# Performance work log

Hardware: AMD Instinct MI355X
Metric: run time of the kernel (lower is better)

Reference implementation:

```python
import jax, jax.numpy as jnp
import numpy as np

B = 4; IN_CH = 256; HEAD_CH = 64; NUM_CLS = 3; H = 128; W = 128
NH = 4; KEY = 16; VAL = 16; OUT_CH = 2
VX = 0.1 * 8; VY = 0.1 * 8  # voxel_size[:2] * out_size_factor
DW = 1.6; DL = 3.9; STRIDE = 1
C_CTR = (HEAD_CH + 2 + NUM_CLS) * 9      # 621
C_COR = (HEAD_CH + 2 + NUM_CLS * 4) * 8  # 624
C_FG = (HEAD_CH + 2 + NUM_CLS) * 9       # 621


def _sampler_points():
    offs = np.arange(-STRIDE, STRIDE + 1, STRIDE, dtype=np.float32)
    oy, ox = np.meshgrid(offs, offs, indexing='ij')
    ctr = np.stack([ox, oy], 0).reshape(2, 9)  # pixel offsets
    cx = np.array([-DW/2, -DW/2, DW/2, DW/2, DL/2, -DL/2, DL/2, -DL/2], np.float32) / VX
    cy = np.array([DL/2, -DL/2, DL/2, -DL/2, -DW/2, -DW/2, DW/2, DW/2], np.float32) / VY
    # faithful to torch: stack(dim=1) -> [8,2] then .view(2,8) (row-major reinterpret)
    cor = np.stack([cx, cy], 1).reshape(2, 8)
    r = max(DW, DL)
    fx = np.array([-r/3, -r/3, -r/3, 0, 0, 0, r/3, r/3, r/3], np.float32) / VX
    fy = np.array([-r/3, 0, r/3, -r/3, 0, r/3, -r/3, 0, r/3], np.float32) / VY
    fg = np.stack([fx, fy], 1).reshape(2, 9)
    return jnp.asarray(ctr), jnp.asarray(cor), jnp.asarray(fg)


def _raw_grid():
    gx = jnp.arange(W, dtype=jnp.float32) + 0.5
    gy = jnp.arange(H, dtype=jnp.float32) + 0.5
    return jnp.stack([jnp.broadcast_to(gx[None, :], (H, W)),
                      jnp.broadcast_to(gy[:, None], (H, W))], 0)  # [2,H,W]


def _conv3x3(x, w, b):
    y = jax.lax.conv_general_dilated(x, w, (1, 1), 'SAME',
                                     dimension_numbers=('NCHW', 'OIHW', 'NCHW'))
    return y + b[None, :, None, None]


def _cbr3(x, w, b, s, t):  # conv3x3 + inference-mode BN (folded scale/shift) + relu
    return jax.nn.relu(_conv3x3(x, w, b) * s[None, :, None, None] + t[None, :, None, None])


def _cbr1(x, w, b, s, t):  # per-head 1x1 conv + BN + relu, w: [NH,O,C], x: [B,C,H,W]
    y = jnp.einsum('noc,bchw->nbohw', w, x) + b[:, None, :, None, None]
    return jax.nn.relu(y * s[:, None, :, None, None] + t[:, None, :, None, None])


def _sample(feats, grids):
    # feats [B,C,H,W]; grids [2,n,H,W] pixel coords. Matches F.grid_sample
    # (bilinear, zeros padding, align_corners=False): sample at pixel coord g-0.5.
    n = grids.shape[1]
    geo = jnp.stack([grids[0] / W, grids[1] / H], 0)  # recover_coords, [2,n,H,W]
    gx, gy = grids[0] - 0.5, grids[1] - 0.5
    x0f = jnp.floor(gx); y0f = jnp.floor(gy)
    dx, dy = gx - x0f, gy - y0f
    x0 = x0f.astype(jnp.int32); y0 = y0f.astype(jnp.int32)
    flat = feats.reshape(B, -1, H * W)

    def gather(xc, yc, wgt):
        valid = ((xc >= 0) & (xc < W) & (yc >= 0) & (yc < H)).astype(feats.dtype) * wgt
        idx = jnp.clip(yc, 0, H - 1) * W + jnp.clip(xc, 0, W - 1)
        v = jnp.take(flat, idx.reshape(-1), axis=2).reshape(B, -1, n, H, W)
        return v * valid[None, None]

    s = (gather(x0, y0, (1 - dx) * (1 - dy)) + gather(x0 + 1, y0, dx * (1 - dy))
         + gather(x0, y0 + 1, (1 - dx) * dy) + gather(x0 + 1, y0 + 1, dx * dy))
    geo_b = jnp.broadcast_to(geo[None], (B,) + geo.shape)
    out = jnp.concatenate([s, geo_b], axis=1)  # [B,C+2,n,H,W]
    return out.reshape(B, -1, H, W)           # channel index = c*n + p, as torch .view


def _forward(base_feats, cc_w, cc_b, cc_s, cc_t, ch_w, ch_b,
             oc_w, oc_b, oc_s, oc_t, oh_w, oh_b,
             fc_w, fc_b, fc_s, fc_t, fh_w, fh_b,
             q_w, q_b, q_s, q_t,
             ck_w, ck_b, ck_s, ck_t, cv_w, cv_b, cv_s, cv_t,
             kk_w, kk_b, kk_s, kk_t, kv_w, kv_b, kv_s, kv_t,
             fk_w, fk_b, fk_s, fk_t, fv_w, fv_b, fv_s, fv_t,
             p1_w, p1_b, p1_s, p1_t, p2_w, p2_b):
    center_feat = _cbr3(base_feats, cc_w, cc_b, cc_s, cc_t)
    center_map = _conv3x3(center_feat, ch_w, ch_b)
    corner_feat = _cbr3(base_feats, oc_w, oc_b, oc_s, oc_t)
    corner_map = _conv3x3(corner_feat, oh_w, oh_b)
    fg_feat = _cbr3(base_feats, fc_w, fc_b, fc_s, fc_t)
    fg_map = _conv3x3(fg_feat, fh_w, fh_b)

    ctr_pts, cor_pts, fg_pts = _sampler_points()
    raw = _raw_grid()
    g_ctr = raw[:, None] + ctr_pts[:, :, None, None]  # [2,9,H,W]
    g_cor = raw[:, None] + cor_pts[:, :, None, None]  # [2,8,H,W]
    g_fg = raw[:, None] + fg_pts[:, :, None, None]    # [2,9,H,W]

    cs = _sample(jnp.concatenate([center_feat, center_map], 1), g_ctr)  # [B,621,H,W]
    os_ = _sample(jnp.concatenate([corner_feat, corner_map], 1), g_cor)  # [B,624,H,W]
    fs = _sample(jnp.concatenate([fg_feat, fg_map], 1), g_fg)            # [B,621,H,W]

    q = _cbr1(base_feats, q_w, q_b, q_s, q_t)  # [NH,B,KEY,H,W]
    ck = _cbr1(cs, ck_w, ck_b, ck_s, ck_t); cv = _cbr1(cs, cv_w, cv_b, cv_s, cv_t)
    ok = _cbr1(os_, kk_w, kk_b, kk_s, kk_t); ov = _cbr1(os_, kv_w, kv_b, kv_s, kv_t)
    fk = _cbr1(fs, fk_w, fk_b, fk_s, fk_t); fv = _cbr1(fs, fv_w, fv_b, fv_s, fv_t)

    logits = jnp.stack([(q * ck).sum(2), (q * ok).sum(2), (q * fk).sum(2)], axis=2)  # [NH,B,3,H,W]
    attw = jax.nn.softmax(logits, axis=2)
    vals = jnp.stack([cv, ov, fv], axis=2)          # [NH,B,3,VAL,H,W]
    att = (attw[:, :, :, None] * vals).sum(2)       # [NH,B,VAL,H,W]

    # predict: 1x1 conv over cat([base_feats, att]) + BN + relu, then 1x1 to out_ch
    h1 = (jnp.einsum('noc,bchw->nbohw', p1_w[:, :, :IN_CH], base_feats)
          + jnp.einsum('nov,nbvhw->nbohw', p1_w[:, :, IN_CH:], att)
          + p1_b[:, None, :, None, None])
    h1 = jax.nn.relu(h1 * p1_s[:, None, :, None, None] + p1_t[:, None, :, None, None])
    pred = jnp.einsum('npo,nbohw->nbphw', p2_w, h1) + p2_b[:, None, :, None, None]
    heads = jnp.moveaxis(pred, 0, 1).reshape(B, NH * OUT_CH, H, W)
    return jnp.concatenate([center_map, corner_map, fg_map, heads], axis=1)  # [B,26,H,W]


def setup_inputs() -> dict:
    ks = iter(jax.random.split(jax.random.key(0), 80))

    def rn(shape, s=0.05):
        return jax.random.normal(next(ks), shape, jnp.float32) * s

    d = {"base_feats": jax.random.normal(next(ks), (B, IN_CH, H, W), jnp.float32)}
    for conv, head, hc in (("cc", "ch", NUM_CLS), ("oc", "oh", NUM_CLS * 4), ("fc", "fh", NUM_CLS)):
        d[conv + "_w"] = rn((HEAD_CH, IN_CH, 3, 3)); d[conv + "_b"] = rn((HEAD_CH,))
        d[conv + "_s"] = 1.0 + rn((HEAD_CH,)); d[conv + "_t"] = rn((HEAD_CH,))
        d[head + "_w"] = rn((hc, HEAD_CH, 3, 3)); d[head + "_b"] = jnp.full((hc,), -2.19, jnp.float32)
    d["q_w"] = rn((NH, KEY, IN_CH)); d["q_b"] = rn((NH, KEY))
    d["q_s"] = 1.0 + rn((NH, KEY)); d["q_t"] = rn((NH, KEY))
    for name, cin, cout in (("ck", C_CTR, KEY), ("cv", C_CTR, VAL), ("kk", C_COR, KEY),
                            ("kv", C_COR, VAL), ("fk", C_FG, KEY), ("fv", C_FG, VAL)):
        d[name + "_w"] = rn((NH, cout, cin)); d[name + "_b"] = rn((NH, cout))
        d[name + "_s"] = 1.0 + rn((NH, cout)); d[name + "_t"] = rn((NH, cout))
    d["p1_w"] = rn((NH, HEAD_CH, IN_CH + VAL)); d["p1_b"] = rn((NH, HEAD_CH))
    d["p1_s"] = 1.0 + rn((NH, HEAD_CH)); d["p1_t"] = rn((NH, HEAD_CH))
    d["p2_w"] = rn((NH, OUT_CH, HEAD_CH)); d["p2_b"] = jnp.full((NH, OUT_CH), -2.19, jnp.float32)
    return d


def reference(base_feats, cc_w, cc_b, cc_s, cc_t, ch_w, ch_b,
              oc_w, oc_b, oc_s, oc_t, oh_w, oh_b,
              fc_w, fc_b, fc_s, fc_t, fh_w, fh_b,
              q_w, q_b, q_s, q_t,
              ck_w, ck_b, ck_s, ck_t, cv_w, cv_b, cv_s, cv_t,
              kk_w, kk_b, kk_s, kk_t, kv_w, kv_b, kv_s, kv_t,
              fk_w, fk_b, fk_s, fk_t, fv_w, fv_b, fv_s, fv_t,
              p1_w, p1_b, p1_s, p1_t, p2_w, p2_b):
    return _forward(base_feats, cc_w, cc_b, cc_s, cc_t, ch_w, ch_b,
                    oc_w, oc_b, oc_s, oc_t, oh_w, oh_b,
                    fc_w, fc_b, fc_s, fc_t, fh_w, fh_b,
                    q_w, q_b, q_s, q_t,
                    ck_w, ck_b, ck_s, ck_t, cv_w, cv_b, cv_s, cv_t,
                    kk_w, kk_b, kk_s, kk_t, kv_w, kv_b, kv_s, kv_t,
                    fk_w, fk_b, fk_s, fk_t, fv_w, fv_b, fv_s, fv_t,
                    p1_w, p1_b, p1_s, p1_t, p2_w, p2_b)
```

## Files before the change

### kernel.cpp

```cpp
#include <hip/hip_runtime.h>
#include <hip/hip_bf16.h>
#include <math.h>


#define HW 16384
#define WIMG 128

typedef unsigned short ushortT;
typedef __attribute__((ext_vector_type(8))) short short8;
typedef __attribute__((ext_vector_type(4))) float floatx4;
typedef __attribute__((ext_vector_type(4))) unsigned uintx4;

constexpr size_t OFF_KV    = 16777216;
constexpr size_t OFF_A16   = 29360128;
constexpr size_t OFF_B16   = 38012928;
constexpr size_t OFF_CWT   = 46057216;
constexpr size_t OFF_CB    = OFF_CWT + 221184;
constexpr size_t OFF_HWT   = OFF_CB + 192;
constexpr size_t OFF_QWT   = OFF_HWT + 13824;
constexpr size_t OFF_QB    = OFF_QWT + 8192;
constexpr size_t OFF_KVW   = OFF_QB + 64;
constexpr size_t OFF_GEO   = OFF_KVW + 266240;
constexpr size_t OFF_P1WT  = OFF_GEO + 1152;
constexpr size_t OFF_P1B   = OFF_P1WT + 40960;

struct P53 { const float* p[53]; };

__device__ inline ushortT f2bf(float f) {
    unsigned u = __float_as_uint(f);
    unsigned r = (u + 0x7FFFu + ((u >> 16) & 1u)) >> 16;
    return (ushortT)r;
}
__device__ inline unsigned packbf(float a, float b) {
    return (unsigned)f2bf(a) | ((unsigned)f2bf(b) << 16);
}
__device__ inline float bf2f(ushortT u) {
    return __uint_as_float((unsigned)u << 16);
}

typedef __attribute__((address_space(3))) ushortT lds_us;
typedef __attribute__((address_space(1))) const ushortT glb_us;
__device__ inline void gload_lds16(const ushortT* g, ushortT* ldsbase) {
    __builtin_amdgcn_global_load_lds((glb_us*)g, (lds_us*)ldsbase, 16, 0, 0);
}

__device__ const float c_ox[3][9] = {
    {-1.f, 0.f, 1.f, -1.f, 0.f, 1.f, -1.f, 0.f, 1.f},
    {-1.f, 2.4375f, -1.f, -2.4375f, 1.f, 2.4375f, 1.f, -2.4375f, 0.f},
    {-1.625f, -1.625f, -1.625f, 0.f, -1.625f, 1.625f, 0.f, -1.625f, 0.f}};
__device__ const float c_oy[3][9] = {
    {-1.f, -1.f, -1.f, 0.f, 0.f, 0.f, 1.f, 1.f, 1.f},
    {2.4375f, -1.f, -2.4375f, -1.f, 2.4375f, 1.f, -2.4375f, 1.f, 0.f},
    {0.f, 0.f, 1.625f, 1.625f, -1.625f, 1.625f, 0.f, 1.625f, 1.625f}};

__device__ const int tapX_cor[16] = {-1,-1, 2, 3,-1,-1,-3,-2, 1, 1, 2, 3, 1, 1,-3,-2};
__device__ const int tapY_cor[16] = { 2, 3,-1,-1,-3,-2,-1,-1, 2, 3, 1, 1,-3,-2, 1, 1};
__device__ const int tapR_cor[16] = { 4, 5, 2, 2, 0, 1, 2, 2, 4, 5, 3, 3, 0, 1, 3, 3};

__device__ inline float cornw(float off, int X) {
    float f = floorf(off);
    float d = off - f;
    int fi = (int)f;
    return (X == fi) ? (1.f - d) : (X == fi + 1) ? d : 0.f;
}

__global__ __launch_bounds__(256) void setup_kernel(P53 ptrs, float* __restrict__ ws,
                                                    const float* __restrict__ base,
                                                    ushortT* __restrict__ a16,
                                                    ushortT* __restrict__ b16) {
    int i = blockIdx.x * 256 + threadIdx.x;
    const float* const* p = ptrs.p;
    if (i < 1102464) {
        if (i < 442368) {
            int tap = i / 49152, r = i % 49152;
            int g = r / 1536, r2 = r % 1536;
            int M = r2 >> 3, j = r2 & 7;
            int br = M >> 6, oc = M & 63, ic = g * 8 + j;
            float v = p[1 + 6 * br][(oc * 256 + ic) * 9 + tap] * p[3 + 6 * br][oc];
            ((ushortT*)(ws + OFF_CWT))[i] = f2bf(v);
            return;
        }
        i -= 442368;
        if (i < 192) {
            int br = i >> 6, oc = i & 63;
            ws[OFF_CB + i] = p[2 + 6 * br][oc] * p[3 + 6 * br][oc] + p[4 + 6 * br][oc];
            return;
        }
        i -= 192;
        if (i < 27648) {
            int j = i & 7, m = (i >> 3) & 15, u = (i >> 7) % 72, br = i / 9216;
            int cnt = (br == 1) ? 12 : 3;
            int t = u >> 3, g = u & 7, ic = g * 8 + j;
            const float* hw = (br == 0) ? p[5] : (br == 1) ? p[11] : p[17];
            float v = (m < cnt) ? hw[(m * 64 + ic) * 9 + t] : 0.f;
            ((ushortT*)(ws + OFF_HWT))[i] = f2bf(v);
            return;
        }
        i -= 27648;
        if (i < 16384) {
            int j = i & 7, m = (i >> 3) & 63, sg = i >> 9;
            int k = (sg >> 2) * 32 + (sg & 3) * 8 + j;
            ((ushortT*)(ws + OFF_QWT))[i] = f2bf(p[19][m * 256 + k] * p[21][m]);
            return;
        }
        i -= 16384;
        if (i < 64) { ws[OFF_QB + i] = p[20][i] * p[21][i] + p[22][i]; return; }
        i -= 64;
        if (i < 532480) {
            int br, NQ, NTAP, n, C, i2;
            if (i < 110592)      { br = 0; NQ = 3; NTAP = 9;  n = 9; C = 67; i2 = i; }
            else if (i < 274432) { br = 1; NQ = 4; NTAP = 16; n = 8; C = 76; i2 = i - 110592; }
            else                 { br = 2; NQ = 7; NTAP = 25; n = 9; C = 67; i2 = i - 274432; }
            int gsz = NQ * 4096;
            int g = i2 / gsz, r = i2 % gsz;
            int q = r >> 12, r2 = r & 4095;
            int sub = r2 >> 10, m = (r2 >> 3) & 127, j = r2 & 7;
            int t = q * 4 + sub, c = g * 8 + j;
            float v = 0.f;
            if (t < NTAP && c < C) {
                int X, Y;
                if (br == 0)      { X = t % 3 - 1; Y = t / 3 - 1; }
                else if (br == 1) { X = tapX_cor[t]; Y = tapY_cor[t]; }
                else              { X = t % 5 - 2; Y = t / 5 - 2; }
                const float* wsrc = (m < 64) ? p[23 + 8 * br] : p[27 + 8 * br];
                int mo = (m < 64) ? m : m - 64;
                float sc = (m < 64) ? p[25 + 8 * br][mo] : p[29 + 8 * br][mo];
                int Cn = (C + 2) * n;
                float s = 0.f;
                for (int pp = 0; pp < n; ++pp) {
                    float ww = cornw(c_ox[br][pp], X) * cornw(c_oy[br][pp], Y);
                    if (ww != 0.f) s += ww * wsrc[mo * Cn + c * n + pp];
                }
                v = s * sc;
            }
            ((ushortT*)(ws + OFF_KVW))[i] = f2bf(v);
            return;
        }
        i -= 532480;
        if (i < 1152) {
            int br = i / 384, rem = i % 384, which = rem >> 7, m = rem & 127;
            int n = (br == 1) ? 8 : 9, C = (br == 1) ? 76 : 67, Cn = (C + 2) * n;
            const float* wsrc = (m < 64) ? p[23 + 8 * br] : p[27 + 8 * br];
            int mo = (m < 64) ? m : m - 64;
            float sc = (m < 64) ? p[25 + 8 * br][mo] : p[29 + 8 * br][mo];
            float bb = (m < 64) ? p[24 + 8 * br][mo] : p[28 + 8 * br][mo];
            float tt = (m < 64) ? p[26 + 8 * br][mo] : p[30 + 8 * br][mo];
            float v = 0.f;
            if (which == 0) {
                for (int pp = 0; pp < n; ++pp) v += wsrc[mo * Cn + C * n + pp];
                v *= sc;
            } else if (which == 1) {
                for (int pp = 0; pp < n; ++pp) v += wsrc[mo * Cn + (C + 1) * n + pp];
                v *= sc;
            } else {
                for (int pp = 0; pp < n; ++pp)
                    v += wsrc[mo * Cn + C * n + pp] * c_ox[br][pp]
                       + wsrc[mo * Cn + (C + 1) * n + pp] * c_oy[br][pp];
                v = v * sc * 0.0078125f + bb * sc + tt;
            }
            ws[OFF_GEO + br * 384 + which * 128 + m] = v;
            return;
        }
        i -= 1152;
        if (i < 81920) {
            int j = i & 7, M = (i >> 3) & 255, sg = i >> 11;
            int k = (sg >> 2) * 32 + (sg & 3) * 8 + j;
            int nh = M >> 6, oc = M & 63;
            float sc = p[49][nh * 64 + oc];
            float v;
            if (k < 256) v = p[47][(nh * 64 + oc) * 272 + k] * sc;
            else {
                int k2 = k - 256, nh2 = k2 >> 4, va = k2 & 15;
                v = (nh2 == nh) ? p[47][(nh * 64 + oc) * 272 + 256 + va] * sc : 0.f;
            }
            ((ushortT*)(ws + OFF_P1WT))[i] = f2bf(v);
            return;
        }
        i -= 81920;
        if (i < 256) { ws[OFF_P1B + i] = p[48][i] * p[49][i] + p[50][i]; }
        return;
    }
    int idx = i - 1102464;
    if (idx < 4 * 32 * 130 * 130) {
        int col = idx % 130, t = idx / 130;
        int row = t % 130; t /= 130;
        int icg = t & 31, b = t >> 5;
        int h = row - 1, w = col - 1;
        unsigned wds[4] = {0u, 0u, 0u, 0u};
        if ((unsigned)h < 128u && (unsigned)w < 128u) {
            const float* s = base + (size_t)(b * 256 + icg * 8) * HW + h * WIMG + w;
            #pragma unroll
            for (int jp = 0; jp < 4; ++jp)
                wds[jp] = packbf(s[(size_t)(2 * jp) * HW], s[(size_t)(2 * jp + 1) * HW]);
        }
        unsigned* d = (unsigned*)(a16 + (size_t)idx * 8);
        d[0] = wds[0]; d[1] = wds[1]; d[2] = wds[2]; d[3] = wds[3];
        return;
    }
    idx -= 4 * 32 * 130 * 130;
    if (idx < 4 * 28 * 134 * 134) {
        int col = idx % 134, row = (idx / 134) % 134;
        if (row < 3 || row >= 131 || col < 3 || col >= 131) {
            unsigned* d = (unsigned*)(b16 + (size_t)idx * 8);
            d[0] = 0u; d[1] = 0u; d[2] = 0u; d[3] = 0u;
        }
    }
}

__global__ __launch_bounds__(256) void conv_base_mfma(
    const ushortT* __restrict__ a16, const ushortT* __restrict__ wA,
    const float* __restrict__ cb, ushortT* __restrict__ b16)
{
    const int wv = threadIdx.x >> 6, lane = threadIdx.x & 63;
    const int sub = lane >> 4, ln = lane & 15;
    const int xh = blockIdx.x, h = blockIdx.y, b = blockIdx.z;
    const int x0 = xh * 64;
    __shared__ __align__(16) ushortT sbuf[2][792 * 8];

    floatx4 acc[3][4];
    #pragma unroll
    for (int mt = 0; mt < 3; ++mt)
        #pragma unroll
        for (int nt = 0; nt < 4; ++nt)
            #pragma unroll
            for (int r = 0; r < 4; ++r) acc[mt][nt][r] = 0.f;

    const int wbase = threadIdx.x & ~63;
    auto stage = [&](int s, int buf) {
        #pragma unroll
        for (int it = 0; it < 4; ++it) {
            int idx = threadIdx.x + it * 256;
            if (idx < 792) {
                int col = idx % 66, t2 = idx / 66;
                int r = t2 % 3, icg = t2 / 3;
                const ushortT* g = a16 +
                    (((size_t)(b * 32 + s * 4 + icg) * 130 + (h + r)) * 130 + (x0 + col)) * 8;
                gload_lds16(g, &sbuf[buf][(size_t)(it * 256 + wbase) * 8]);
            }
        }
    };
    stage(0, 0);
    for (int s = 0; s < 8; ++s) {
        __syncthreads();
        if (s < 7) stage(s + 1, (s + 1) & 1);
        const ushortT* sb = sbuf[s & 1];
        #pragma unroll
        for (int tap = 0; tap < 9; ++tap) {
            const int ky = tap / 3, kx = tap % 3;
            short8 Bf[4];
            #pragma unroll
            for (int nt = 0; nt < 4; ++nt) {
                int c = nt * 16 + ln + kx;
                Bf[nt] = *(const short8*)(sb + ((sub * 3 + ky) * 66 + c) * 8);
            }
            const int g = s * 4 + sub;
            short8 Af[3];
            #pragma unroll
            for (int mt = 0; mt < 3; ++mt) {
                int m = wv * 48 + mt * 16 + ln;
                Af[mt] = *(const short8*)(wA + (((size_t)tap * 32 + g) * 192 + m) * 8);
            }
            #pragma unroll
            for (int mt = 0; mt < 3; ++mt)
                #pragma unroll
                for (int nt = 0; nt < 4; ++nt)
                    acc[mt][nt] = __builtin_amdgcn_mfma_f32_16x16x32_bf16(
                        Af[mt], Bf[nt], acc[mt][nt], 0, 0, 0);
        }
    }
    #pragma unroll
    for (int mt = 0; mt < 3; ++mt) {
        int ocq = wv * 48 + mt * 16 + sub * 4;
        #pragma unroll
        for (int nt = 0; nt < 4; ++nt) {
            int px = x0 + nt * 16 + ln;
            float v0 = fmaxf(acc[mt][nt][0] + cb[ocq + 0], 0.f);
            float v1 = fmaxf(acc[mt][nt][1] + cb[ocq + 1], 0.f);
            float v2 = fmaxf(acc[mt][nt][2] + cb[ocq + 2], 0.f);
            float v3 = fmaxf(acc[mt][nt][3] + cb[ocq + 3], 0.f);
            unsigned lo = packbf(v0, v1), hi = packbf(v2, v3);
            unsigned plo = (unsigned)__shfl_down((int)lo, 16);
            unsigned phi = (unsigned)__shfl_down((int)hi, 16);
            if (!(sub & 1)) {
                int br = ocq >> 6, oc = ocq & 63;
                int grp = ((br == 0) ? 0 : (br == 1) ? 9 : 19) + (oc >> 3);
                uintx4 w = {lo, hi, plo, phi};
                *(uintx4*)(b16 +
                    (((size_t)(b * 28 + grp) * 134 + (h + 3)) * 134 + (px + 3)) * 8) = w;
            }
        }
    }
}

__global__ __launch_bounds__(256) void conv_head_mfma(
    const ushortT* __restrict__ b16c, const ushortT* __restrict__ wH,
    const float* __restrict__ chb, const float* __restrict__ ohb,
    const float* __restrict__ fhb, float* __restrict__ out,
    ushortT* __restrict__ b16)
{
    const int wv = threadIdx.x >> 6, lane = threadIdx.x & 63;
    const int sub = lane >> 4, ln = lane & 15;
    const int x0 = (blockIdx.x & 1) * 64, h = blockIdx.x >> 1;
    const int br = blockIdx.y % 3, b = blockIdx.y / 3;
    const int cnt = (br == 1) ? 12 : 3;
    const int mapb = (br == 0) ? 0 : (br == 1) ? 3 : 15;
    const int grpb = (br == 0) ? 0 : (br == 1) ? 9 : 19;
    const float* bias = (br == 0) ? chb : (br == 1) ? ohb : fhb;
    __shared__ __align__(16) ushortT sbuf[8 * 3 * 66 * 8];
    const int wbase = threadIdx.x & ~63;

    for (int it = 0; it < 7; ++it) {
        int idx = threadIdx.x + it * 256;
        if (idx < 1584) {
            int col = idx % 66, t2 = idx / 66;
            int r = t2 % 3, g = t2 / 3;
            const ushortT* gp = b16c +
                (((size_t)(b * 28 + grpb + g) * 134 + (h + r + 2)) * 134 + (x0 + col + 2)) * 8;
            gload_lds16(gp, sbuf + (size_t)(it * 256 + wbase) * 8);
        }
    }
    __syncthreads();

    floatx4 acc;
    #pragma unroll
    for (int r = 0; r < 4; ++r) acc[r] = 0.f;
    #pragma unroll
    for (int k = 0; k < 18; ++k) {
        int u = k * 4 + sub;
        int t = u >> 3, g = u & 7;
        int dxv = t % 3 - 1, ry = t / 3;
        short8 Af = *(const short8*)(wH + ((size_t)(br * 72 + u) * 16 + ln) * 8);
        int c = wv * 16 + ln + dxv + 1;
        short8 Bf = *(const short8*)(sbuf + ((g * 3 + ry) * 66 + c) * 8);
        acc = __builtin_amdgcn_mfma_f32_16x16x32_bf16(Af, Bf, acc, 0, 0, 0);
    }
    {
        int px = x0 + wv * 16 + ln;
        #pragma unroll
        for (int r = 0; r < 4; ++r) {
            int m = sub * 4 + r;
            if (m < cnt) {
                float v = acc[r] + bias[m];
                out[((size_t)b * 26 + mapb + m) * HW + h * WIMG + px] = v;
                int grp = grpb + 8 + (m >> 3), j = m & 7;
                b16[(((size_t)(b * 28 + grp) * 134 + (h + 3)) * 134 + (px + 3)) * 8 + j]
                    = f2bf(v);
            }
        }
    }
}

template<int BRV>
__device__ __forceinline__ void kv_body(
    const ushortT* __restrict__ b16, const ushortT* __restrict__ kvw,
    const float* __restrict__ geob, ushortT* __restrict__ kvout,
    ushortT* __restrict__ sbuf)
{
    constexpr int NGRP = (BRV == 0) ? 9 : (BRV == 1) ? 5 : 9;
    constexpr int NPH  = (BRV == 1) ? 2 : 1;
    constexpr int NTAP = (BRV == 0) ? 9 : (BRV == 1) ? 16 : 25;
    constexpr int NQ   = (BRV == 0) ? 3 : (BRV == 1) ? 4 : 7;
    constexpr int ROWS = (BRV == 0) ? 3 : (BRV == 1) ? 6 : 5;
    constexpr int COLS = (BRV == 0) ? 34 : (BRV == 1) ? 38 : 36;
    constexpr int XMIN = (BRV == 0) ? -1 : (BRV == 1) ? -3 : -2;
    constexpr int UBASE = (BRV == 0) ? 0 : (BRV == 1) ? 9 : 19;
    constexpr int NEL  = NGRP * ROWS * COLS;
    constexpr int NIT  = (NEL + 255) / 256;
    constexpr int WBASE = (BRV == 0) ? 0 : (BRV == 1) ? 110592 : 274432;

    const int lane = threadIdx.x & 63, wv = threadIdx.x >> 6;
    const int sub = lane >> 4, ln = lane & 15;
    const int x0 = blockIdx.x * 32, h = blockIdx.y;
    const int b = blockIdx.z & 3;
    const int wbase = threadIdx.x & ~63;
    const int thrB = ln * 16;

    int boff[NQ];
    #pragma unroll
    for (int q = 0; q < NQ; ++q) {
        int t = q * 4 + sub;
        int dxv, ry;
        if (t >= NTAP)          { dxv = -XMIN; ry = 0; }
        else if (BRV == 0)      { dxv = t % 3 - 1; ry = t / 3; }
        else if (BRV == 1)      { dxv = tapX_cor[t]; ry = tapR_cor[t]; }
        else                    { dxv = t % 5 - 2; ry = t / 5; }
        boff[q] = (ry * COLS + (dxv - XMIN)) * 16 + thrB;
    }

    auto stage = [&](int ph) {
        #pragma unroll
        for (int it = 0; it < NIT; ++it) {
            int idx = threadIdx.x + it * 256;
            if (idx < NEL) {
                int grp = idx / (ROWS * COLS), r2 = idx % (ROWS * COLS);
                int rw = r2 / COLS, col = r2 % COLS;
                int dy = (BRV == 1) ? ((rw < 3) ? rw - 3 : rw - 2) : (rw - ROWS / 2);
                const ushortT* gp = b16 +
                    (((size_t)(b * 28 + UBASE + ph * NGRP + grp) * 134 + (h + dy + 3)) * 134
                     + (x0 + col + XMIN + 3)) * 8;
                gload_lds16(gp, sbuf + (size_t)(it * 256 + wbase) * 8);
            }
        }
    };

    floatx4 acc[2][2];
    #pragma unroll
    for (int mt = 0; mt < 2; ++mt)
        #pragma unroll
        for (int nt = 0; nt < 2; ++nt)
            #pragma unroll
            for (int r = 0; r < 4; ++r) acc[mt][nt][r] = 0.f;

    for (int ph = 0; ph < NPH; ++ph) {
        if (ph) __syncthreads();
        stage(ph);
        __syncthreads();
        for (int g = 0; g < NGRP; ++g) {
            const char* sb8 = (const char*)sbuf + g * (ROWS * COLS * 16);
            const ushortT* wg = kvw + WBASE
                + ((size_t)(ph * NGRP + g) * NQ) * 4096 + sub * 1024 + (wv * 32 + ln) * 8;
            short8 A0[2], B0[2], A1[2], B1[2];
            auto ldf = [&](int q, short8 A[2], short8 B[2]) {
                #pragma unroll
                for (int mt = 0; mt < 2; ++mt)
                    A[mt] = *(const short8*)(wg + (size_t)q * 4096 + mt * 128);
                int bb = boff[q];
                #pragma unroll
                for (int nt = 0; nt < 2; ++nt)
                    B[nt] = *(const short8*)(sb8 + bb + nt * 256);
            };
            auto dom = [&](short8 A[2], short8 B[2]) {
                #pragma unroll
                for (int mt = 0; mt < 2; ++mt)
                    #pragma unroll
                    for (int nt = 0; nt < 2; ++nt)
                        acc[mt][nt] = __builtin_amdgcn_mfma_f32_16x16x32_bf16(
                            A[mt], B[nt], acc[mt][nt], 0, 0, 0);
            };
            ldf(0, A0, B0);
            #pragma unroll
            for (int q = 0; q < NQ; q += 2) {
                bool h1 = (q + 1 < NQ);
                if (h1) ldf(q + 1, A1, B1);
                dom(A0, B0);
                if (q + 2 < NQ) ldf(q + 2, A0, B0);
                if (h1) dom(A1, B1);
            }
        }
    }

    const float* geo = geob + BRV * 384;
    const float fy = (h + 0.5f) * 0.0078125f;
    #pragma unroll
    for (int mt = 0; mt < 2; ++mt)
        #pragma unroll
        for (int nt = 0; nt < 2; ++nt) {
            int px = x0 + nt * 16 + ln;
            float fx = (px + 0.5f) * 0.0078125f;
            #pragma unroll
            for (int r = 0; r < 4; ++r) {
                int Mi = wv * 32 + mt * 16 + sub * 4 + r;
                float v = acc[mt][nt][r] + geo[Mi] * fx + geo[128 + Mi] * fy + geo[256 + Mi];
                kvout[((size_t)(BRV * 4 + b) * 128 + Mi) * HW + h * WIMG + px] =
                    f2bf(fmaxf(v, 0.f));
            }
        }
}

__global__ __launch_bounds__(256, 6) void kv_all3(
    const ushortT* __restrict__ b16, const ushortT* __restrict__ kvw,
    const float* __restrict__ geob, ushortT* __restrict__ kvout)
{
    __shared__ __align__(16) ushortT sbuf[1620 * 8];
    const int brv = blockIdx.z >> 2;
    if (brv == 0)      kv_body<0>(b16, kvw, geob, kvout, sbuf);
    else if (brv == 1) kv_body<1>(b16, kvw, geob, kvout, sbuf);
    else               kv_body<2>(b16, kvw, geob, kvout, sbuf);
}

__global__ __launch_bounds__(256) void attn_pred_mfma(
    float* __restrict__ ws, const float* __restrict__ p2w,
    const float* __restrict__ p2b, float* __restrict__ out)
{
    const int wv = threadIdx.x >> 6, lane = threadIdx.x & 63;
    const int sub = lane >> 4, ln = lane & 15;
    const int px0 = blockIdx.x * 64, b = blockIdx.y;
    const ushortT* wP1 = (const ushortT*)(ws + OFF_P1WT);
    const ushortT* wQ  = (const ushortT*)(ws + OFF_QWT);
    const ushortT* a16 = (const ushortT*)(ws + OFF_A16);
    const ushortT* kv = (const ushortT*)(ws + OFF_KV);
    const float* p1b = ws + OFF_P1B;
    const float* qb  = ws + OFF_QB;
    __shared__ __align__(16) ushortT xbuf[40 * 64 * 8];
    __shared__ __align__(16) ushortT qld[64 * 64];

    const int mypx = threadIdx.x & 63, nh = threadIdx.x >> 6;
    const int gpx = px0 + mypx, hh = gpx >> 7, ww = gpx & 127;
    #pragma unroll
    for (int g2 = 0; g2 < 8; ++g2) {
        int g = nh * 8 + g2;
        const ushortT* gp = a16 +
            (((size_t)(b * 32 + g) * 130 + (hh + 1)) * 130 + (ww + 1)) * 8;
        gload_lds16(gp, xbuf + (size_t)g * 64 * 8);
    }
    __syncthreads();

    {
        floatx4 qacc[4];
        #pragma unroll
        for (int nt = 0; nt < 4; ++nt)
            #pragma unroll
            for (int r = 0; r < 4; ++r) qacc[nt][r] = 0.f;
        #pragma unroll
        for (int kk = 0; kk < 8; ++kk) {
            short8 Af = *(const short8*)(wQ + (((kk * 4 + sub) * 64) + wv * 16 + ln) * 8);
            #pragma unroll
            for (int nt = 0; nt < 4; ++nt) {
                short8 Bf = *(const short8*)(xbuf + (((kk * 4 + sub) * 64) + nt * 16 + ln) * 8);
                qacc[nt] = __builtin_amdgcn_mfma_f32_16x16x32_bf16(Af, Bf, qacc[nt], 0, 0, 0);
            }
        }
        #pragma unroll
        for (int nt = 0; nt < 4; ++nt)
            #pragma unroll
            for (int r = 0; r < 4; ++r) {
                int row = wv * 16 + sub * 4 + r;
                qld[row * 64 + nt * 16 + ln] = f2bf(fmaxf(qacc[nt][r] + qb[row], 0.f));
            }
    }
    __syncthreads();

    {
        float l[3];
        #pragma unroll
        for (int br = 0; br < 3; ++br) {
            float s = 0.f;
            #pragma unroll
            for (int ko = 0; ko < 16; ++ko)
                s = fmaf(bf2f(qld[(nh * 16 + ko) * 64 + mypx]),
                         bf2f(kv[(size_t)((br * 4 + b) * 128 + nh * 16 + ko) * HW + gpx]), s);
            l[br] = s;
        }
        float m = fmaxf(l[0], fmaxf(l[1], l[2]));
        float e0 = __expf(l[0] - m), e1 = __expf(l[1] - m), e2 = __expf(l[2] - m);
        float inv = 1.f / (e0 + e1 + e2);
        float aw0 = e0 * inv, aw1 = e1 * inv, aw2 = e2 * inv;
        #pragma unroll
        for (int vap = 0; vap < 8; ++vap) {
            int va0 = vap * 2, va1 = vap * 2 + 1;
            float a0 =
                aw0 * bf2f(kv[(size_t)((0 * 4 + b) * 128 + 64 + nh * 16 + va0) * HW + gpx]) +
                aw1 * bf2f(kv[(size_t)((1 * 4 + b) * 128 + 64 + nh * 16 + va0) * HW + gpx]) +
                aw2 * bf2f(kv[(size_t)((2 * 4 + b) * 128 + 64 + nh * 16 + va0) * HW + gpx]);
            float a1 =
                aw0 * bf2f(kv[(size_t)((0 * 4 + b) * 128 + 64 + nh * 16 + va1) * HW + gpx]) +
                aw1 * bf2f(kv[(size_t)((1 * 4 + b) * 128 + 64 + nh * 16 + va1) * HW + gpx]) +
                aw2 * bf2f(kv[(size_t)((2 * 4 + b) * 128 + 64 + nh * 16 + va1) * HW + gpx]);
            int g = 32 + nh * 2 + (vap >> 2), wo = vap & 3;
            ((unsigned*)xbuf)[(g * 64 + mypx) * 4 + wo] = packbf(a0, a1);
        }
    }
    __syncthreads();

    floatx4 acc[4][4];
    #pragma unroll
    for (int mt = 0; mt < 4; ++mt)
        #pragma unroll
        for (int nt = 0; nt < 4; ++nt)
            #pragma unroll
            for (int r = 0; r < 4; ++r) acc[mt][nt][r] = 0.f;
    #pragma unroll
    for (int kk = 0; kk < 10; ++kk) {
        short8 Bf[4];
        #pragma unroll
        for (int nt = 0; nt < 4; ++nt)
            Bf[nt] = *(const short8*)(xbuf + (((kk * 4 + sub) * 64) + nt * 16 + ln) * 8);
        #pragma unroll
        for (int mt = 0; mt < 4; ++mt) {
            short8 Af = *(const short8*)(wP1 +
                (((size_t)(kk * 4 + sub) * 256) + wv * 64 + mt * 16 + ln) * 8);
            #pragma unroll
            for (int nt = 0; nt < 4; ++nt)
                acc[mt][nt] = __builtin_amdgcn_mfma_f32_16x16x32_bf16(Af, Bf[nt], acc[mt][nt], 0, 0, 0);
        }
    }

    float po0[4] = {0.f, 0.f, 0.f, 0.f}, po1[4] = {0.f, 0.f, 0.f, 0.f};
    #pragma unroll
    for (int mt = 0; mt < 4; ++mt)
        #pragma unroll
        for (int r = 0; r < 4; ++r) {
            int oc = mt * 16 + sub * 4 + r;
            float bias = p1b[wv * 64 + oc];
            float w0 = p2w[(wv * 2 + 0) * 64 + oc];
            float w1 = p2w[(wv * 2 + 1) * 64 + oc];
            #pragma unroll
            for (int nt = 0; nt < 4; ++nt) {
                float hv = fmaxf(acc[mt][nt][r] + bias, 0.f);
                po0[nt] = fmaf(w0, hv, po0[nt]);
                po1[nt] = fmaf(w1, hv, po1[nt]);
            }
        }
    #pragma unroll
    for (int nt = 0; nt < 4; ++nt) {
        po0[nt] += __shfl_xor(po0[nt], 16);
        po0[nt] += __shfl_xor(po0[nt], 32);
        po1[nt] += __shfl_xor(po1[nt], 16);
        po1[nt] += __shfl_xor(po1[nt], 32);
    }
    if (sub == 0) {
        #pragma unroll
        for (int nt = 0; nt < 4; ++nt) {
            int px = px0 + nt * 16 + ln;
            out[((size_t)b * 26 + 18 + wv * 2 + 0) * HW + px] = po0[nt] + p2b[wv * 2 + 0];
            out[((size_t)b * 26 + 18 + wv * 2 + 1) * HW + px] = po1[nt] + p2b[wv * 2 + 1];
        }
    }
}

extern "C" void kernel_launch(void* const* d_in, const int* in_sizes, int n_in,
                              void* d_out, int out_size, void* d_ws, size_t ws_size,
                              hipStream_t stream) {
    (void)in_sizes; (void)n_in; (void)out_size; (void)ws_size;
    float* ws  = (float*)d_ws;
    float* out = (float*)d_out;
    const float* base = (const float*)d_in[0];
    P53 ptrs;
    for (int i = 0; i < 53; ++i) ptrs.p[i] = (const float*)d_in[i];

    ushortT* a16 = (ushortT*)(ws + OFF_A16);
    ushortT* b16 = (ushortT*)(ws + OFF_B16);
    ushortT* kvb = (ushortT*)(ws + OFF_KV);
    const ushortT* kvw = (const ushortT*)(ws + OFF_KVW);

    setup_kernel<<<20613, 256, 0, stream>>>(ptrs, ws, base, a16, b16);
    conv_base_mfma<<<dim3(2, 128, 4), 256, 0, stream>>>(
        a16, (const ushortT*)(ws + OFF_CWT), ws + OFF_CB, b16);
    conv_head_mfma<<<dim3(256, 12), 256, 0, stream>>>(
        b16, (const ushortT*)(ws + OFF_HWT),
        (const float*)d_in[6], (const float*)d_in[12], (const float*)d_in[18],
        out, b16);
    kv_all3<<<dim3(4, 128, 12), 256, 0, stream>>>(b16, kvw, ws + OFF_GEO, kvb);
    attn_pred_mfma<<<dim3(256, 4), 256, 0, stream>>>(ws, (const float*)d_in[51],
                                                     (const float*)d_in[52], out);
}
```

Before: 436.4 us.

## Widen kv kernel tile to full image row, stage one group at a time

The kv conv kernel now has each block compute a full 128-pixel row instead of a 32-pixel strip. Each weight A-fragment load is reused across 8 N-tiles instead of 2, and the halo overhead on staged columns shrinks. LDS staging now holds one channel group at a time with a barrier per group, replacing multi-group phases, which cuts shared memory use. The grid drops to 1536 blocks with a lower occupancy hint and more accumulator registers. That reduces parallelism and adds synchronisation, and the explicit double-buffered prefetch of fragments is removed.

```diff
diff --git a/kernel.cpp b/kernel.cpp
--- a/kernel.cpp
+++ b/kernel.cpp
@@ -354,24 +354,21 @@
 __device__ __forceinline__ void kv_body(
     const ushortT* __restrict__ b16, const ushortT* __restrict__ kvw,
     const float* __restrict__ geob, ushortT* __restrict__ kvout,
-    ushortT* __restrict__ sbuf)
+    ushortT* __restrict__ sbuf, int h, int b)
 {
-    constexpr int NGRP = (BRV == 0) ? 9 : (BRV == 1) ? 5 : 9;
-    constexpr int NPH  = (BRV == 1) ? 2 : 1;
+    constexpr int NG   = (BRV == 0) ? 9 : (BRV == 1) ? 10 : 9;
     constexpr int NTAP = (BRV == 0) ? 9 : (BRV == 1) ? 16 : 25;
     constexpr int NQ   = (BRV == 0) ? 3 : (BRV == 1) ? 4 : 7;
     constexpr int ROWS = (BRV == 0) ? 3 : (BRV == 1) ? 6 : 5;
-    constexpr int COLS = (BRV == 0) ? 34 : (BRV == 1) ? 38 : 36;
+    constexpr int COLS = (BRV == 0) ? 130 : (BRV == 1) ? 134 : 132;
     constexpr int XMIN = (BRV == 0) ? -1 : (BRV == 1) ? -3 : -2;
     constexpr int UBASE = (BRV == 0) ? 0 : (BRV == 1) ? 9 : 19;
-    constexpr int NEL  = NGRP * ROWS * COLS;
+    constexpr int NEL  = ROWS * COLS;
     constexpr int NIT  = (NEL + 255) / 256;
     constexpr int WBASE = (BRV == 0) ? 0 : (BRV == 1) ? 110592 : 274432;
 
     const int lane = threadIdx.x & 63, wv = threadIdx.x >> 6;
     const int sub = lane >> 4, ln = lane & 15;
-    const int x0 = blockIdx.x * 32, h = blockIdx.y;
-    const int b = blockIdx.z & 3;
     const int wbase = threadIdx.x & ~63;
     const int thrB = ln * 16;
 
@@ -387,64 +384,47 @@
         boff[q] = (ry * COLS + (dxv - XMIN)) * 16 + thrB;
     }
 
-    auto stage = [&](int ph) {
+    auto stage = [&](int g) {
         #pragma unroll
         for (int it = 0; it < NIT; ++it) {
             int idx = threadIdx.x + it * 256;
             if (idx < NEL) {
-                int grp = idx / (ROWS * COLS), r2 = idx % (ROWS * COLS);
-                int rw = r2 / COLS, col = r2 % COLS;
+                int rw = idx / COLS, col = idx % COLS;
                 int dy = (BRV == 1) ? ((rw < 3) ? rw - 3 : rw - 2) : (rw - ROWS / 2);
                 const ushortT* gp = b16 +
-                    (((size_t)(b * 28 + UBASE + ph * NGRP + grp) * 134 + (h + dy + 3)) * 134
-                     + (x0 + col + XMIN + 3)) * 8;
+                    (((size_t)(b * 28 + UBASE + g) * 134 + (h + dy + 3)) * 134
+                     + (col + XMIN + 3)) * 8;
                 gload_lds16(gp, sbuf + (size_t)(it * 256 + wbase) * 8);
             }
         }
     };
 
-    floatx4 acc[2][2];
+    floatx4 acc[2][8];
     #pragma unroll
     for (int mt = 0; mt < 2; ++mt)
         #pragma unroll
-        for (int nt = 0; nt < 2; ++nt)
+        for (int nt = 0; nt < 8; ++nt)
             #pragma unroll
             for (int r = 0; r < 4; ++r) acc[mt][nt][r] = 0.f;
 
-    for (int ph = 0; ph < NPH; ++ph) {
-        if (ph) __syncthreads();
-        stage(ph);
+    const ushortT* wp0 = kvw + WBASE + (size_t)sub * 1024 + (wv * 32 + ln) * 8;
+
+    for (int g = 0; g < NG; ++g) {
+        if (g) __syncthreads();
+        stage(g);
         __syncthreads();
-        for (int g = 0; g < NGRP; ++g) {
-            const char* sb8 = (const char*)sbuf + g * (ROWS * COLS * 16);
-            const ushortT* wg = kvw + WBASE
-                + ((size_t)(ph * NGRP + g) * NQ) * 4096 + sub * 1024 + (wv * 32 + ln) * 8;
-            short8 A0[2], B0[2], A1[2], B1[2];
-            auto ldf = [&](int q, short8 A[2], short8 B[2]) {
-                #pragma unroll
-                for (int mt = 0; mt < 2; ++mt)
-                    A[mt] = *(const short8*)(wg + (size_t)q * 4096 + mt * 128);
-                int bb = boff[q];
-                #pragma unroll
-                for (int nt = 0; nt < 2; ++nt)
-                    B[nt] = *(const short8*)(sb8 + bb + nt * 256);
-            };
-            auto dom = [&](short8 A[2], short8 B[2]) {
-                #pragma unroll
-                for (int mt = 0; mt < 2; ++mt)
-                    #pragma unroll
-                    for (int nt = 0; nt < 2; ++nt)
-                        acc[mt][nt] = __builtin_amdgcn_mfma_f32_16x16x32_bf16(
-                            A[mt], B[nt], acc[mt][nt], 0, 0, 0);
-            };
-            ldf(0, A0, B0);
-            #pragma unroll
-            for (int q = 0; q < NQ; q += 2) {
-                bool h1 = (q + 1 < NQ);
-                if (h1) ldf(q + 1, A1, B1);
-                dom(A0, B0);
-                if (q + 2 < NQ) ldf(q + 2, A0, B0);
-                if (h1) dom(A1, B1);
+        const char* sb8 = (const char*)sbuf;
+        const ushortT* wg = wp0 + (size_t)g * (NQ * 4096);
+        #pragma unroll
+        for (int q = 0; q < NQ; ++q) {
+            short8 A0 = *(const short8*)(wg + (size_t)q * 4096);
+            short8 A1 = *(const short8*)(wg + (size_t)q * 4096 + 128);
+            int bb = boff[q];
+            #pragma unroll
+            for (int nt = 0; nt < 8; ++nt) {
+                short8 Bf = *(const short8*)(sb8 + bb + nt * 256);
+                acc[0][nt] = __builtin_amdgcn_mfma_f32_16x16x32_bf16(A0, Bf, acc[0][nt], 0, 0, 0);
+                acc[1][nt] = __builtin_amdgcn_mfma_f32_16x16x32_bf16(A1, Bf, acc[1][nt], 0, 0, 0);
             }
         }
     }
@@ -454,8 +434,8 @@
     #pragma unroll
     for (int mt = 0; mt < 2; ++mt)
         #pragma unroll
-        for (int nt = 0; nt < 2; ++nt) {
-            int px = x0 + nt * 16 + ln;
+        for (int nt = 0; nt < 8; ++nt) {
+            int px = nt * 16 + ln;
             float fx = (px + 0.5f) * 0.0078125f;
             #pragma unroll
             for (int r = 0; r < 4; ++r) {
@@ -467,15 +447,17 @@
         }
 }
 
-__global__ __launch_bounds__(256, 6) void kv_all3(
+__global__ __launch_bounds__(256, 4) void kv_all4(
     const ushortT* __restrict__ b16, const ushortT* __restrict__ kvw,
     const float* __restrict__ geob, ushortT* __restrict__ kvout)
 {
-    __shared__ __align__(16) ushortT sbuf[1620 * 8];
-    const int brv = blockIdx.z >> 2;
-    if (brv == 0)      kv_body<0>(b16, kvw, geob, kvout, sbuf);
-    else if (brv == 1) kv_body<1>(b16, kvw, geob, kvout, sbuf);
-    else               kv_body<2>(b16, kvw, geob, kvout, sbuf);
+    __shared__ __align__(16) ushortT sbuf[804 * 8];
+    const int h = blockIdx.x;
+    const int z = blockIdx.y;
+    const int brv = z >> 2, b = z & 3;
+    if (brv == 0)      kv_body<0>(b16, kvw, geob, kvout, sbuf, h, b);
+    else if (brv == 1) kv_body<1>(b16, kvw, geob, kvout, sbuf, h, b);
+    else               kv_body<2>(b16, kvw, geob, kvout, sbuf, h, b);
 }
 
 __global__ __launch_bounds__(256) void attn_pred_mfma(
@@ -640,7 +622,7 @@
         b16, (const ushortT*)(ws + OFF_HWT),
         (const float*)d_in[6], (const float*)d_in[12], (const float*)d_in[18],
         out, b16);
-    kv_all3<<<dim3(4, 128, 12), 256, 0, stream>>>(b16, kvw, ws + OFF_GEO, kvb);
+    kv_all4<<<dim3(128, 12), 256, 0, stream>>>(b16, kvw, ws + OFF_GEO, kvb);
     attn_pred_mfma<<<dim3(256, 4), 256, 0, stream>>>(ws, (const float*)d_in[51],
                                                      (const float*)d_in[52], out);
 }
```

New measurement: 424.0 us. 2.8% less time.
